# Optimization experiments

Measured on AMD Instinct MI355X. Metric: run time of the kernel, lower is better.

## Reference

```python
import jax, jax.numpy as jnp
import numpy as np

E, O, I = 8, 512, 1024  # num_experts, out_features, in_features
TOK_PER_EXPERT = 8192
T = E * TOK_PER_EXPERT  # total routed tokens


def setup_inputs() -> dict:
    key = jax.random.key(0)
    k1, k2 = jax.random.split(key)
    inputs = jax.random.normal(k1, (T, I), dtype=jnp.float32)
    # Learned per-expert weights, shape (E, O, I) as in GraniteMoeParallelExperts
    weight = jax.random.normal(k2, (E, O, I), dtype=jnp.float32) * (1.0 / np.sqrt(I))
    return {"inputs": inputs, "weight": weight, "expert_size": TOK_PER_EXPERT}


def reference(inputs, weight, expert_size):
    # inputs: [T, I] tokens sorted by expert; expert_size tokens per expert (static).
    # Equivalent to: split(inputs, expert_size) -> per-expert x @ W_e^T -> concat.
    e, o, i = weight.shape
    x = inputs.reshape(e, expert_size, i)          # [E, S, I]
    out = jnp.einsum('esi,eoi->eso', x, weight)    # grouped GEMM, [E, S, O]
    return out.reshape(e * expert_size, o)         # [T, O]
```

## Files before the change

kernel.cpp:

```cpp
#include <hip/hip_runtime.h>
#include <hip/hip_bf16.h>


#define NE 8
#define NO 512
#define NI 1024
#define NS 8192

#define BM 128
#define BK 32
#define NT (NI / BK)
#define LDA 40

typedef __attribute__((ext_vector_type(4))) float f32x4;
typedef __attribute__((ext_vector_type(4))) short s16x4;
typedef __attribute__((ext_vector_type(8))) short s16x8;

__device__ __forceinline__ s16x4 cvt4(f32x4 a) {
    s16x4 r;
    r[0] = (short)__builtin_bit_cast(unsigned short, __float2bfloat16(a[0]));
    r[1] = (short)__builtin_bit_cast(unsigned short, __float2bfloat16(a[1]));
    r[2] = (short)__builtin_bit_cast(unsigned short, __float2bfloat16(a[2]));
    r[3] = (short)__builtin_bit_cast(unsigned short, __float2bfloat16(a[3]));
    return r;
}

__global__ __launch_bounds__(256)
void pack_w(const float* __restrict__ W, short* __restrict__ Wpk) {
    int idx  = blockIdx.x * 256 + threadIdx.x;
    int l    = idx & 63;
    int kt32 = (idx >> 6) & 31;
    int g    = (idx >> 11) & 31;
    int e    = idx >> 16;
    const float* src = W + (size_t)(e * NO + g * 16 + (l & 15)) * NI
                         + kt32 * 32 + (l >> 4) * 8;
    f32x4 a = *(const f32x4*)src;
    f32x4 b = *(const f32x4*)(src + 4);
    s16x4 lo = cvt4(a), hi = cvt4(b);
    s16x8 r;
    r[0] = lo[0]; r[1] = lo[1]; r[2] = lo[2]; r[3] = lo[3];
    r[4] = hi[0]; r[5] = hi[1]; r[6] = hi[2]; r[7] = hi[3];
    *(s16x8*)(Wpk + (size_t)idx * 8) = r;
}

__global__ __launch_bounds__(512, 1)
void moe_gemm(const float* __restrict__ X,
              const short* __restrict__ Wpk,
              float* __restrict__ Out) {
    int bid  = blockIdx.x;
    int e    = bid & 7;
    int mblk = bid >> 3;

    const float* Ap = X   + ((size_t)e * NS + (size_t)mblk * BM) * NI;
    const short* Bp = Wpk + (size_t)e * (32 * 32 * 64 * 8);
    float*       Cp = Out + ((size_t)e * NS + (size_t)mblk * BM) * NO;

    __shared__ short lA[2][BM * LDA];

    const int tid  = threadIdx.x;
    const int lane = tid & 63;
    const int wn   = tid >> 6;
    const int l15  = lane & 15;
    const int lhi  = lane >> 4;

    f32x4 acc[8][4];
#pragma unroll
    for (int i = 0; i < 8; ++i)
#pragma unroll
        for (int j = 0; j < 4; ++j)
            acc[i][j] = (f32x4){0.f, 0.f, 0.f, 0.f};

    f32x4 ar[2];
    s16x8 bfA[4], bfB[4], af[8];

#define AISSUE(kt)                                                             \
    do {                                                                       \
        _Pragma("unroll") for (int i = 0; i < 2; ++i) {                        \
            int u = tid + i * 512;                                             \
            ar[i] = *(const f32x4*)(Ap + (size_t)(u >> 3) * NI +               \
                                    (kt) * BK + (u & 7) * 4);                  \
        }                                                                      \
    } while (0)

#define AWRITE(buf)                                                            \
    do {                                                                       \
        _Pragma("unroll") for (int i = 0; i < 2; ++i) {                        \
            int u = tid + i * 512;                                             \
            *(s16x4*)&lA[buf][(u >> 3) * LDA + (u & 7) * 4] = cvt4(ar[i]);     \
        }                                                                      \
    } while (0)

#define BLOAD(kt, dst)                                                         \
    do {                                                                       \
        _Pragma("unroll") for (int ni = 0; ni < 4; ++ni)                       \
            dst[ni] = *(const s16x8*)(Bp +                                     \
                ((size_t)((wn * 4 + ni) * 32 + (kt)) * 64 + lane) * 8);        \
    } while (0)

#define READA(c)                                                               \
    do {                                                                       \
        _Pragma("unroll") for (int mi = 0; mi < 8; ++mi)                       \
            af[mi] = *(const s16x8*)&lA[c][(mi * 16 + l15) * LDA + lhi * 8];   \
    } while (0)

#define MFMA(bf)                                                               \
    do {                                                                       \
        __builtin_amdgcn_s_setprio(1);                                         \
        _Pragma("unroll") for (int mi = 0; mi < 8; ++mi)                       \
            _Pragma("unroll") for (int ni = 0; ni < 4; ++ni)                   \
                acc[mi][ni] = __builtin_amdgcn_mfma_f32_16x16x32_bf16(         \
                    af[mi], bf[ni], acc[mi][ni], 0, 0, 0);                     \
        __builtin_amdgcn_s_setprio(0);                                         \
    } while (0)

#define BAR()   __builtin_amdgcn_s_barrier()
#define LGKM0() asm volatile("s_waitcnt lgkmcnt(0)" ::: "memory")
#define VM(n)   asm volatile("s_waitcnt vmcnt(" #n ")" ::: "memory")

    AISSUE(0);
    VM(0);
    AWRITE(0);
    BLOAD(0, bfA);
    AISSUE(1);
    BLOAD(1, bfB);
    VM(6);
    LGKM0();
    BAR();

#define TILE_MAIN(kt, bfc)                                                     \
    do {                                                                       \
        VM(4);                         \
        AWRITE(((kt) + 1) & 1);                                                \
        AISSUE((kt) + 2);                                                      \
        READA((kt) & 1);                                                       \
        MFMA(bfc);                                                             \
        BLOAD((kt) + 2, bfc);                  \
        LGKM0();                                                               \
        BAR();                                                                 \
    } while (0)

#pragma unroll 1
    for (int kt2 = 0; kt2 < NT / 2 - 1; ++kt2) {
        const int kt = kt2 * 2;
        TILE_MAIN(kt, bfA);
        TILE_MAIN(kt + 1, bfB);
    }
    {
        VM(4);
        AWRITE(1);
        READA(0);
        MFMA(bfA);
        LGKM0();
        BAR();
        VM(0);
        READA(1);
        MFMA(bfB);
    }

#pragma unroll
    for (int mi = 0; mi < 8; ++mi) {
#pragma unroll
        for (int rr = 0; rr < 4; ++rr) {
            int row   = mi * 16 + lhi * 4 + rr;
            float* cp = Cp + (size_t)row * NO + wn * 64 + l15;
#pragma unroll
            for (int ni = 0; ni < 4; ++ni)
                cp[ni * 16] = acc[mi][ni][rr];
        }
    }
#undef AISSUE
#undef AWRITE
#undef BLOAD
#undef READA
#undef MFMA
#undef TILE_MAIN
#undef BAR
#undef LGKM0
#undef VM
}

extern "C" void kernel_launch(void* const* d_in, const int* in_sizes, int n_in,
                              void* d_out, int out_size, void* d_ws, size_t ws_size,
                              hipStream_t stream) {
    const float* X = (const float*)d_in[0];
    const float* W = (const float*)d_in[1];
    float* Out     = (float*)d_out;
    short* Wpk     = (short*)d_ws;

    hipLaunchKernelGGL(pack_w, dim3(2048), dim3(256), 0, stream, W, Wpk);
    hipLaunchKernelGGL(moe_gemm, dim3(NE * (NS / BM)), dim3(512), 0,
                       stream, X, Wpk, Out);
}
```

Before: 116.8 us.

## Double the K-tile to 64 with XOR-swizzled LDS and a restructured prefetch pipeline

Raises the A-tile depth from 32 to 64, so each LDS stage now feeds two MFMA rounds that use the two B-fragment register sets. Row padding of LDS is replaced by an XOR swizzle to avoid bank conflicts. The main loop is rewritten so each B prefetch is issued right after its MFMA round, with vmcnt waits adjusted to match. The goal is to halve the number of barriers and LDS write phases per K and to deepen global-load overlap. The cost is more A registers held in flight and a different wait ordering.

```diff
diff --git a/kernel.cpp b/kernel.cpp
--- a/kernel.cpp
+++ b/kernel.cpp
@@ -8,9 +8,8 @@
 #define NS 8192
 
 #define BM 128
-#define BK 32
-#define NT (NI / BK)
-#define LDA 40
+#define BK 64
+#define NP (NI / BK)
 
 typedef __attribute__((ext_vector_type(4))) float f32x4;
 typedef __attribute__((ext_vector_type(4))) short s16x4;
@@ -55,7 +54,7 @@
     const short* Bp = Wpk + (size_t)e * (32 * 32 * 64 * 8);
     float*       Cp = Out + ((size_t)e * NS + (size_t)mblk * BM) * NO;
 
-    __shared__ short lA[2][BM * LDA];
+    __shared__ short lA[2][BM * BK];
 
     const int tid  = threadIdx.x;
     const int lane = tid & 63;
@@ -70,23 +69,26 @@
         for (int j = 0; j < 4; ++j)
             acc[i][j] = (f32x4){0.f, 0.f, 0.f, 0.f};
 
-    f32x4 ar[2];
+    f32x4 ar[4];
     s16x8 bfA[4], bfB[4], af[8];
 
-#define AISSUE(kt)                                                             \
+#define AISSUE(p)                                                              \
     do {                                                                       \
-        _Pragma("unroll") for (int i = 0; i < 2; ++i) {                        \
+        _Pragma("unroll") for (int i = 0; i < 4; ++i) {                        \
             int u = tid + i * 512;                                             \
-            ar[i] = *(const f32x4*)(Ap + (size_t)(u >> 3) * NI +               \
-                                    (kt) * BK + (u & 7) * 4);                  \
+            ar[i] = *(const f32x4*)(Ap + (size_t)(u >> 4) * NI +               \
+                                    (p) * BK + (u & 15) * 4);                  \
         }                                                                      \
     } while (0)
 
 #define AWRITE(buf)                                                            \
     do {                                                                       \
-        _Pragma("unroll") for (int i = 0; i < 2; ++i) {                        \
-            int u = tid + i * 512;                                             \
-            *(s16x4*)&lA[buf][(u >> 3) * LDA + (u & 7) * 4] = cvt4(ar[i]);     \
+        _Pragma("unroll") for (int i = 0; i < 4; ++i) {                        \
+            int u    = tid + i * 512;                                          \
+            int row  = u >> 4;                                                 \
+            int c4   = u & 15;                                                 \
+            int phys = (c4 >> 1) ^ (row & 7);                                  \
+            *(s16x4*)&lA[buf][row * BK + phys * 8 + (c4 & 1) * 4] = cvt4(ar[i]); \
         }                                                                      \
     } while (0)
 
@@ -97,10 +99,13 @@
                 ((size_t)((wn * 4 + ni) * 32 + (kt)) * 64 + lane) * 8);        \
     } while (0)
 
-#define READA(c)                                                               \
+#define READA(c, kk)                                                           \
     do {                                                                       \
-        _Pragma("unroll") for (int mi = 0; mi < 8; ++mi)                       \
-            af[mi] = *(const s16x8*)&lA[c][(mi * 16 + l15) * LDA + lhi * 8];   \
+        _Pragma("unroll") for (int mi = 0; mi < 8; ++mi) {                     \
+            int r  = mi * 16 + l15;                                            \
+            af[mi] = *(const s16x8*)&lA[c][r * BK +                            \
+                                           ((((kk) * 4 + lhi) ^ (r & 7)) << 3)]; \
+        }                                                                      \
     } while (0)
 
 #define MFMA(bf)                                                               \
@@ -121,41 +126,33 @@
     VM(0);
     AWRITE(0);
     BLOAD(0, bfA);
+    BLOAD(1, bfB);
     AISSUE(1);
-    BLOAD(1, bfB);
-    VM(6);
     LGKM0();
     BAR();
 
-#define TILE_MAIN(kt, bfc)                                                     \
-    do {                                                                       \
-        VM(4);                         \
-        AWRITE(((kt) + 1) & 1);                                                \
-        AISSUE((kt) + 2);                                                      \
-        READA((kt) & 1);                                                       \
-        MFMA(bfc);                                                             \
-        BLOAD((kt) + 2, bfc);                  \
-        LGKM0();                                                               \
-        BAR();                                                                 \
-    } while (0)
-
 #pragma unroll 1
-    for (int kt2 = 0; kt2 < NT / 2 - 1; ++kt2) {
-        const int kt = kt2 * 2;
-        TILE_MAIN(kt, bfA);
-        TILE_MAIN(kt + 1, bfB);
-    }
-    {
+    for (int j = 0; j < NP - 1; ++j) {
+        const int c = j & 1;
         VM(4);
-        AWRITE(1);
-        READA(0);
+        READA(c, 0);
         MFMA(bfA);
+        BLOAD(2 * j + 2, bfA);
+        READA(c, 1);
+        MFMA(bfB);
+        BLOAD(2 * j + 3, bfB);
+        VM(8);
+        AWRITE(c ^ 1);
+        if (j < NP - 2) AISSUE(j + 2);
         LGKM0();
         BAR();
-        VM(0);
-        READA(1);
-        MFMA(bfB);
     }
+    VM(4);
+    READA(1, 0);
+    MFMA(bfA);
+    VM(0);
+    READA(1, 1);
+    MFMA(bfB);
 
 #pragma unroll
     for (int mi = 0; mi < 8; ++mi) {
@@ -173,7 +170,6 @@
 #undef BLOAD
 #undef READA
 #undef MFMA
-#undef TILE_MAIN
 #undef BAR
 #undef LGKM0
 #undef VM
```

Result: faster. 114.1 us (median of 3 runs) (-2.3%).
